# Optimization experiments

Hardware: AMD Instinct MI355X
Metric: run time of the kernel (lower is better)

## Reference

```python
import jax, jax.numpy as jnp
import numpy as np

N = 100000   # nodes
E = 1600000  # edges
D = 128      # input_dim
H = 128      # hidden_dim
G = 1000     # num graphs
C = 10       # output_dim
EPS = 1e-5   # BatchNorm eps


def setup_inputs() -> dict:
    key = jax.random.key(0)
    ks = jax.random.split(key, 16)
    inp = {
        "x": jax.random.normal(ks[0], (N, D), dtype=jnp.float32),
        "edge_index": jax.random.randint(ks[1], (2, E), 0, N, dtype=jnp.int64),
        "batch": jnp.sort(jax.random.randint(ks[2], (N,), 0, G, dtype=jnp.int64)),
    }
    s_in, s_h = 1.0 / np.sqrt(D), 1.0 / np.sqrt(H)
    inp["W1"] = jax.random.normal(ks[3], (D, H), jnp.float32) * s_in
    inp["b1"] = jnp.zeros((H,), jnp.float32)
    inp["W2"] = jax.random.normal(ks[4], (H, H), jnp.float32) * s_h
    inp["b2"] = jnp.zeros((H,), jnp.float32)
    inp["W3"] = jax.random.normal(ks[5], (H, H), jnp.float32) * s_h
    inp["b3"] = jnp.zeros((H,), jnp.float32)
    for i in range(1, 4):
        inp[f"g{i}"] = jnp.ones((H,), jnp.float32)
        inp[f"be{i}"] = jnp.zeros((H,), jnp.float32)
    inp["Wc1"] = jax.random.normal(ks[6], (H, H // 2), jnp.float32) * s_h
    inp["bc1"] = jnp.zeros((H // 2,), jnp.float32)
    inp["Wc2"] = jax.random.normal(ks[7], (H // 2, C), jnp.float32) * (1.0 / np.sqrt(H // 2))
    inp["bc2"] = jnp.zeros((C,), jnp.float32)
    return inp


def _edge_norm(edge_index, num_nodes):
    # PyG GCNConv default: add self-loops, symmetric D^-1/2 A D^-1/2 normalization
    loop = jnp.arange(num_nodes, dtype=edge_index.dtype)
    src = jnp.concatenate([edge_index[0], loop])
    dst = jnp.concatenate([edge_index[1], loop])
    deg = jax.ops.segment_sum(jnp.ones_like(dst, dtype=jnp.float32), dst,
                              num_segments=num_nodes)
    dinv = jnp.where(deg > 0, deg ** -0.5, 0.0)
    norm = dinv[src] * dinv[dst]  # [E + N]
    return src, dst, norm


def _gcn_conv(x, W, b, src, dst, norm, num_nodes):
    h = x @ W                              # [N, H]
    msg = h[src] * norm[:, None]           # gather over edges (incl. self-loops)
    out = jax.ops.segment_sum(msg, dst, num_segments=num_nodes)
    return out + b


def _bn_eval(x, gamma, beta):
    # eval-mode BatchNorm1d with running_mean=0, running_var=1 buffers
    return gamma * x * (1.0 / np.sqrt(1.0 + EPS)) + beta


def reference(x, edge_index, batch,
              W1, b1, W2, b2, W3, b3,
              g1, be1, g2, be2, g3, be3,
              Wc1, bc1, Wc2, bc2):
    num_nodes = x.shape[0]
    src, dst, norm = _edge_norm(edge_index, num_nodes)
    h = x
    for (W, b, g, be) in ((W1, b1, g1, be1), (W2, b2, g2, be2), (W3, b3, g3, be3)):
        h = _gcn_conv(h, W, b, src, dst, norm, num_nodes)
        h = jax.nn.relu(_bn_eval(h, g, be))  # dropout is identity in eval mode
    # global_mean_pool over graph ids
    sums = jax.ops.segment_sum(h, batch, num_segments=G)
    cnts = jax.ops.segment_sum(jnp.ones((num_nodes,), h.dtype), batch, num_segments=G)
    pooled = sums / jnp.maximum(cnts, 1.0)[:, None]
    # classifier MLP
    z = jax.nn.relu(pooled @ Wc1 + bc1)
    return z @ Wc2 + bc2
```

## Files before the change

### kernel.cpp

```cpp
#include <hip/hip_runtime.h>
#include <hip/hip_bf16.h>

#define INV1P 0.9999950000374997f
#define BCAP 16384
#define CSRCAP 20480

typedef __attribute__((ext_vector_type(8))) short bfrag;
typedef __attribute__((ext_vector_type(4))) float f32x4;

static __device__ __forceinline__ unsigned bf16rne(float f) {
    unsigned u = __float_as_uint(f);
    return (u + 0x7fffu + ((u >> 16) & 1u)) >> 16;
}
static __device__ __forceinline__ float bflo(unsigned u) { return __uint_as_float(u << 16); }
static __device__ __forceinline__ float bfhi(unsigned u) { return __uint_as_float(u & 0xffff0000u); }


__global__ __launch_bounds__(256) void k_binA(const int* __restrict__ src, const int* __restrict__ dst,
                                              int* __restrict__ gcursor, unsigned* __restrict__ binned, int e) {
    __shared__ unsigned pk[8192];
    __shared__ unsigned char bk[8192];
    __shared__ int hist[256];
    __shared__ int base[256];
    int tid = threadIdx.x;
    hist[tid] = 0;
    __syncthreads();
    int cbase = blockIdx.x * 8192;
    int cnt = min(8192, e - cbase);
    for (int j = tid; j < cnt; j += 256) {
        int s = src[cbase + j], d = dst[cbase + j];
        unsigned b = (unsigned)d >> 9;
        pk[j] = (unsigned)s | (((unsigned)d & 511u) << 17);
        bk[j] = (unsigned char)b;
        atomicAdd(&hist[b], 1);
    }
    __syncthreads();
    int h = hist[tid];
    base[tid] = (h > 0) ? atomicAdd(&gcursor[tid], h) : 0;
    hist[tid] = 0;
    __syncthreads();
    for (int j = tid; j < cnt; j += 256) {
        unsigned b = bk[j];
        int off = atomicAdd(&hist[b], 1);
        binned[base[b] + off] = pk[j];
    }
}

__global__ __launch_bounds__(256) void k_binB2(const unsigned* __restrict__ binned,
                                               const int* __restrict__ gcursor,
                                               int* __restrict__ rowptr, int* __restrict__ rowend,
                                               float* __restrict__ dinv,
                                               int* __restrict__ csr_src, int n, int dummy) {
    __shared__ int cur[512];
    __shared__ int lrp[512];
    __shared__ int ssum[256];
    int b = blockIdx.x, tid = threadIdx.x;
    int nstart = b << 9;
    int nn = min(512, n - nstart);
    int cntb = gcursor[b] - b * BCAP;
    int s0 = b * BCAP, s1 = s0 + cntb;
    int cb = b * CSRCAP;
    cur[tid] = 0; cur[tid + 256] = 0;
    __syncthreads();
    for (int j = s0 + tid; j < s1; j += 256)
        atomicAdd(&cur[(binned[j] >> 17) & 511], 1);
    __syncthreads();
    int c0 = cur[2 * tid], c1 = cur[2 * tid + 1];
    int p0 = (c0 + 7) & ~7, p1 = (c1 + 7) & ~7;
    int pair = p0 + p1;
    ssum[tid] = pair;
    __syncthreads();
    for (int off = 1; off < 256; off <<= 1) {
        int t2 = (tid >= off) ? ssum[tid - off] : 0;
        __syncthreads();
        ssum[tid] += t2;
        __syncthreads();
    }
    int e0 = ssum[tid] - pair;
    int e1 = e0 + p0;
    int st0 = cb + e0, st1 = cb + e1;
    lrp[2 * tid] = st0;
    lrp[2 * tid + 1] = st1;
    if (2 * tid < nn) {
        rowptr[nstart + 2 * tid] = st0;
        rowend[nstart + 2 * tid] = st0 + p0;
        dinv[nstart + 2 * tid] = rsqrtf((float)(c0 + 1));
    }
    if (2 * tid + 1 < nn) {
        rowptr[nstart + 2 * tid + 1] = st1;
        rowend[nstart + 2 * tid + 1] = st1 + p1;
        dinv[nstart + 2 * tid + 1] = rsqrtf((float)(c1 + 1));
    }
    for (int k = c0; k < p0; k++) csr_src[st0 + k] = dummy;
    for (int k = c1; k < p1; k++) csr_src[st1 + k] = dummy;
    cur[2 * tid] = 0; cur[2 * tid + 1] = 0;
    __syncthreads();
    for (int j = s0 + tid; j < s1; j += 256) {
        unsigned p = binned[j];
        int nl = (p >> 17) & 511;
        int idx = atomicAdd(&cur[nl], 1);
        csr_src[lrp[nl] + idx] = p & 0x1ffff;
    }
}


static __device__ __forceinline__ void prepw_body(const float* __restrict__ W, uint4* __restrict__ Bf, int blk) {
    int id = blk * 256 + threadIdx.x;
    int lane = id & 63;
    int e = id >> 6;
    int kk = e >> 3, c = e & 7;
    int kbase = kk * 32 + (lane >> 4) * 8;
    int col = c * 16 + (lane & 15);
    unsigned hi[8], lo[8];
    #pragma unroll
    for (int j = 0; j < 8; j++) {
        float w = W[(kbase + j) * 128 + col];
        unsigned h = bf16rne(w);
        float rh = __uint_as_float(h << 16);
        unsigned l = bf16rne(w - rh);
        hi[j] = h; lo[j] = l;
    }
    uint4 H = make_uint4(hi[0] | (hi[1] << 16), hi[2] | (hi[3] << 16),
                         hi[4] | (hi[5] << 16), hi[6] | (hi[7] << 16));
    uint4 L = make_uint4(lo[0] | (lo[1] << 16), lo[2] | (lo[3] << 16),
                         lo[4] | (lo[5] << 16), lo[6] | (lo[7] << 16));
    Bf[e * 64 + lane] = H;
    Bf[2048 + e * 64 + lane] = L;
}

__global__ __launch_bounds__(256) void k_prep(const float* __restrict__ W1, const float* __restrict__ W2,
                                              const float* __restrict__ W3,
                                              uint4* __restrict__ Bf1, uint4* __restrict__ Bf2,
                                              uint4* __restrict__ Bf3,
                                              int* __restrict__ gcursor,
                                              unsigned* __restrict__ bufA, unsigned* __restrict__ bufB, int n) {
    int b = blockIdx.x;
    if (b < 8)       prepw_body(W1, Bf1, b);
    else if (b < 16) prepw_body(W2, Bf2, b - 8);
    else if (b < 24) prepw_body(W3, Bf3, b - 16);
    else {
        int t = threadIdx.x;
        gcursor[t] = t * BCAP;
        if (t < 64)  bufA[(size_t)n * 64 + t] = 0;
        else if (t < 128) bufB[(size_t)n * 64 + (t - 64)] = 0;
    }
}

static __device__ __forceinline__ void gemm_body(unsigned* __restrict__ Y, const float* __restrict__ dinv,
                                                 int nrows, int rowbase, bfrag* a, uint4* bs) {
    int tid = threadIdx.x;
    int w = tid >> 6, lane = tid & 63;
    __syncthreads();
    f32x4 acc[8];
    #pragma unroll
    for (int c = 0; c < 8; c++) acc[c] = (f32x4){0.f, 0.f, 0.f, 0.f};
    #pragma unroll
    for (int kk = 0; kk < 4; kk++) {
        #pragma unroll
        for (int c = 0; c < 8; c++) {
            bfrag bh = *(const bfrag*)&bs[(kk * 8 + c) * 64 + lane];
            bfrag bl = *(const bfrag*)&bs[2048 + (kk * 8 + c) * 64 + lane];
            acc[c] = __builtin_amdgcn_mfma_f32_16x16x32_bf16(a[kk], bh, acc[c], 0, 0, 0);
            acc[c] = __builtin_amdgcn_mfma_f32_16x16x32_bf16(a[kk], bl, acc[c], 0, 0, 0);
        }
    }
    int rb = rowbase + w * 16 + (lane >> 4) * 4;
    float dv[4];
    #pragma unroll
    for (int r = 0; r < 4; r++) dv[r] = dinv[min(rb + r, nrows - 1)];
    __syncthreads();
    char* epib = (char*)bs;
    ushort* epi = (ushort*)(epib + w * 4352);
    #pragma unroll
    for (int c = 0; c < 8; c++) {
        #pragma unroll
        for (int r = 0; r < 4; r++) {
            int rr = (lane >> 4) * 4 + r;
            epi[rr * 136 + c * 16 + (lane & 15)] = (ushort)bf16rne(acc[c][r] * dv[r]);
        }
    }
    __syncthreads();
    #pragma unroll
    for (int i = 0; i < 4; i++) {
        int id = tid + i * 512;
        int rr = id >> 4, q = id & 15;
        int grow = rowbase + rr;
        if (grow < nrows) {
            uint4 v = *(const uint4*)(epib + (rr >> 4) * 4352 + (rr & 15) * 272 + q * 16);
            ((uint4*)Y)[(size_t)grow * 16 + q] = v;
        }
    }
}

__global__ __launch_bounds__(512) void k_gemm_mfma_f32(const float* __restrict__ X,
                                                       const uint4* __restrict__ Bfr,
                                                       unsigned* __restrict__ Y, const float* __restrict__ dinv,
                                                       int nrows) {
    __shared__ uint4 bs[4096];
    int tid = threadIdx.x;
    int w = tid >> 6, lane = tid & 63;
    int rowbase = blockIdx.x * 128;
    #pragma unroll
    for (int i = 0; i < 8; i++) bs[tid + i * 512] = Bfr[tid + i * 512];
    int row = rowbase + w * 16 + (lane & 15);
    int rowc = min(row, nrows - 1);
    const float4* X4 = (const float4*)X;
    bfrag a[4];
    #pragma unroll
    for (int kk = 0; kk < 4; kk++) {
        float4 f0 = X4[(size_t)rowc * 32 + kk * 8 + (lane >> 4) * 2];
        float4 f1 = X4[(size_t)rowc * 32 + kk * 8 + (lane >> 4) * 2 + 1];
        uint4 av = make_uint4(bf16rne(f0.x) | (bf16rne(f0.y) << 16),
                              bf16rne(f0.z) | (bf16rne(f0.w) << 16),
                              bf16rne(f1.x) | (bf16rne(f1.y) << 16),
                              bf16rne(f1.z) | (bf16rne(f1.w) << 16));
        a[kk] = *(const bfrag*)&av;
    }
    gemm_body(Y, dinv, nrows, rowbase, a, bs);
}

static __device__ __forceinline__ void agg_body(const uint4* __restrict__ H4, int nodec, int l,
                                                const int* __restrict__ rowptr, const int* __restrict__ rowend,
                                                const int* __restrict__ csr_src, float* acc) {
    {
        uint4 hv = H4[(size_t)nodec * 16 + l];
        acc[0] = bflo(hv.x); acc[1] = bfhi(hv.x);
        acc[2] = bflo(hv.y); acc[3] = bfhi(hv.y);
        acc[4] = bflo(hv.z); acc[5] = bfhi(hv.z);
        acc[6] = bflo(hv.w); acc[7] = bfhi(hv.w);
    }
    int s = rowptr[nodec], e = rowend[nodec];
    const int4* csr4 = (const int4*)csr_src;
    int4 ia, ib;
    if (s < e) {
        ia = csr4[(s >> 2)];
        ib = csr4[(s >> 2) + 1];
    }
    for (int j = s; j < e; j += 8) {
        uint4 vv[8];
        vv[0] = H4[(size_t)ia.x * 16 + l];
        vv[1] = H4[(size_t)ia.y * 16 + l];
        vv[2] = H4[(size_t)ia.z * 16 + l];
        vv[3] = H4[(size_t)ia.w * 16 + l];
        vv[4] = H4[(size_t)ib.x * 16 + l];
        vv[5] = H4[(size_t)ib.y * 16 + l];
        vv[6] = H4[(size_t)ib.z * 16 + l];
        vv[7] = H4[(size_t)ib.w * 16 + l];
        int jn = j + 8;
        if (jn < e) {
            ia = csr4[(jn >> 2)];
            ib = csr4[(jn >> 2) + 1];
        }
        #pragma unroll
        for (int q = 0; q < 8; q++) {
            acc[0] += bflo(vv[q].x); acc[1] += bfhi(vv[q].x);
            acc[2] += bflo(vv[q].y); acc[3] += bfhi(vv[q].y);
            acc[4] += bflo(vv[q].z); acc[5] += bfhi(vv[q].z);
            acc[6] += bflo(vv[q].w); acc[7] += bfhi(vv[q].w);
        }
    }
}

static __device__ __forceinline__ void bn_relu(const float* acc, float dn, int l,
                                               const float* __restrict__ bias, const float* __restrict__ gamma,
                                               const float* __restrict__ beta, float* r) {
    float4 bi0 = ((const float4*)bias)[l * 2],  bi1 = ((const float4*)bias)[l * 2 + 1];
    float4 ga0 = ((const float4*)gamma)[l * 2], ga1 = ((const float4*)gamma)[l * 2 + 1];
    float4 be0 = ((const float4*)beta)[l * 2],  be1 = ((const float4*)beta)[l * 2 + 1];
    float g[8] = {ga0.x, ga0.y, ga0.z, ga0.w, ga1.x, ga1.y, ga1.z, ga1.w};
    float bb[8] = {bi0.x, bi0.y, bi0.z, bi0.w, bi1.x, bi1.y, bi1.z, bi1.w};
    float bt[8] = {be0.x, be0.y, be0.z, be0.w, be1.x, be1.y, be1.z, be1.w};
    #pragma unroll
    for (int i = 0; i < 8; i++) {
        float t = g[i] * INV1P;
        r[i] = fmaxf(fmaf(t * dn, acc[i], fmaf(t, bb[i], bt[i])), 0.f);
    }
}

__global__ __launch_bounds__(256) void k_agg_gemm(const uint4* __restrict__ H4,
                                                  const int* __restrict__ rowptr, const int* __restrict__ rowend,
                                                  const int* __restrict__ csr_src,
                                                  const float* __restrict__ dinv,
                                                  const float* __restrict__ bias, const float* __restrict__ gamma,
                                                  const float* __restrict__ beta,
                                                  const uint4* __restrict__ Bfr,
                                                  unsigned* __restrict__ Yn, int nnodes) {
    __shared__ ushort hs[16 * 136];
    int tid = threadIdx.x;
    int nl = tid >> 4;
    int l = tid & 15;
    int base = blockIdx.x * 16;

    {
        int node = base + nl;
        int nodec = min(node, nnodes - 1);
        float acc[8], r[8];
        agg_body(H4, nodec, l, rowptr, rowend, csr_src, acc);
        bn_relu(acc, dinv[nodec], l, bias, gamma, beta, r);
        uint4 o;
        o.x = bf16rne(r[0]) | (bf16rne(r[1]) << 16);
        o.y = bf16rne(r[2]) | (bf16rne(r[3]) << 16);
        o.z = bf16rne(r[4]) | (bf16rne(r[5]) << 16);
        o.w = bf16rne(r[6]) | (bf16rne(r[7]) << 16);
        *(uint4*)&hs[nl * 136 + l * 8] = o;
    }
    __syncthreads();

    int w = tid >> 6, lane = tid & 63;
    int c0 = 2 * w, c1 = 2 * w + 1;
    bfrag a[4];
    #pragma unroll
    for (int kk = 0; kk < 4; kk++)
        a[kk] = *(const bfrag*)&hs[(lane & 15) * 136 + (lane >> 4) * 8 + kk * 32];
    f32x4 ac0 = (f32x4){0.f, 0.f, 0.f, 0.f};
    f32x4 ac1 = (f32x4){0.f, 0.f, 0.f, 0.f};
    #pragma unroll
    for (int kk = 0; kk < 4; kk++) {
        bfrag bh0 = *(const bfrag*)&Bfr[(kk * 8 + c0) * 64 + lane];
        bfrag bl0 = *(const bfrag*)&Bfr[2048 + (kk * 8 + c0) * 64 + lane];
        bfrag bh1 = *(const bfrag*)&Bfr[(kk * 8 + c1) * 64 + lane];
        bfrag bl1 = *(const bfrag*)&Bfr[2048 + (kk * 8 + c1) * 64 + lane];
        ac0 = __builtin_amdgcn_mfma_f32_16x16x32_bf16(a[kk], bh0, ac0, 0, 0, 0);
        ac0 = __builtin_amdgcn_mfma_f32_16x16x32_bf16(a[kk], bl0, ac0, 0, 0, 0);
        ac1 = __builtin_amdgcn_mfma_f32_16x16x32_bf16(a[kk], bh1, ac1, 0, 0, 0);
        ac1 = __builtin_amdgcn_mfma_f32_16x16x32_bf16(a[kk], bl1, ac1, 0, 0, 0);
    }
    __syncthreads();
    #pragma unroll
    for (int r = 0; r < 4; r++) {
        int rowt = (lane >> 4) * 4 + r;
        float dv = dinv[min(base + rowt, nnodes - 1)];
        hs[rowt * 136 + c0 * 16 + (lane & 15)] = (ushort)bf16rne(ac0[r] * dv);
        hs[rowt * 136 + c1 * 16 + (lane & 15)] = (ushort)bf16rne(ac1[r] * dv);
    }
    __syncthreads();
    {
        int row = tid >> 4, q = tid & 15;
        int grow = base + row;
        if (grow < nnodes)
            ((uint4*)Yn)[(size_t)grow * 16 + q] = *(const uint4*)&hs[row * 136 + q * 8];
    }
}

__global__ __launch_bounds__(256) void k_aggregate(const uint4* __restrict__ H4, const int* __restrict__ rowptr,
                                                   const int* __restrict__ rowend,
                                                   const int* __restrict__ csr_src,
                                                   const float* __restrict__ dinv,
                                                   const float* __restrict__ bias, const float* __restrict__ gamma,
                                                   const float* __restrict__ beta,
                                                   uint4* __restrict__ out4, int nnodes) {
    int tid = blockIdx.x * 256 + threadIdx.x;
    int node = tid >> 4;
    int l = tid & 15;
    if (node >= nnodes) return;
    float acc[8], r[8];
    agg_body(H4, node, l, rowptr, rowend, csr_src, acc);
    bn_relu(acc, dinv[node], l, bias, gamma, beta, r);
    uint4 o;
    o.x = bf16rne(r[0]) | (bf16rne(r[1]) << 16);
    o.y = bf16rne(r[2]) | (bf16rne(r[3]) << 16);
    o.z = bf16rne(r[4]) | (bf16rne(r[5]) << 16);
    o.w = bf16rne(r[6]) | (bf16rne(r[7]) << 16);
    out4[(size_t)node * 16 + l] = o;
}

__global__ __launch_bounds__(64) void k_pool(const unsigned* __restrict__ Hf, const int* __restrict__ batch,
                                             float* __restrict__ pooled, float* __restrict__ cnt, int nnodes) {
    int t = threadIdx.x;
    int base = blockIdx.x * 64;
    if (base >= nnodes) return;
    int end = min(base + 64, nnodes);
    float ax = 0.f, ay = 0.f; int run = 0;
    int cur = batch[base];
    for (int i = base; i < end; i++) {
        int bg = batch[i];
        if (bg != cur) {
            atomicAdd(&pooled[(size_t)cur * 128 + 2 * t], ax);
            atomicAdd(&pooled[(size_t)cur * 128 + 2 * t + 1], ay);
            if (t == 0) atomicAdd(&cnt[cur], (float)run);
            ax = 0.f; ay = 0.f; run = 0; cur = bg;
        }
        unsigned u = Hf[(size_t)i * 64 + t];
        ax += bflo(u);
        ay += bfhi(u);
        run++;
    }
    atomicAdd(&pooled[(size_t)cur * 128 + 2 * t], ax);
    atomicAdd(&pooled[(size_t)cur * 128 + 2 * t + 1], ay);
    if (t == 0) atomicAdd(&cnt[cur], (float)run);
}

__global__ __launch_bounds__(64) void k_classifier(const float* __restrict__ pooled, const float* __restrict__ cnt,
                                                   const float* __restrict__ Wc1, const float* __restrict__ bc1,
                                                   const float* __restrict__ Wc2, const float* __restrict__ bc2,
                                                   float* __restrict__ outp, int ngraphs) {
    __shared__ float p[128];
    __shared__ float z[64];
    int g = blockIdx.x;
    int tid = threadIdx.x;
    float inv = 1.0f / fmaxf(cnt[g], 1.0f);
    p[tid]      = pooled[(size_t)g * 128 + tid] * inv;
    p[tid + 64] = pooled[(size_t)g * 128 + 64 + tid] * inv;
    __syncthreads();
    float a = bc1[tid];
    #pragma unroll 8
    for (int k = 0; k < 128; k++) a += p[k] * Wc1[k * 64 + tid];
    z[tid] = fmaxf(a, 0.f);
    __syncthreads();
    if (tid < 10) {
        float o = bc2[tid];
        #pragma unroll 8
        for (int j = 0; j < 64; j++) o += z[j] * Wc2[j * 10 + tid];
        outp[(size_t)g * 10 + tid] = o;
    }
}


static inline size_t align16(size_t v) { return (v + 15) & ~(size_t)15; }

extern "C" void kernel_launch(void* const* d_in, const int* in_sizes, int n_in,
                              void* d_out, int out_size, void* d_ws, size_t ws_size,
                              hipStream_t stream) {
    const float* x      = (const float*)d_in[0];
    const int*   ei     = (const int*)d_in[1];
    const int*   batch  = (const int*)d_in[2];
    const float* W1 = (const float*)d_in[3];  const float* b1 = (const float*)d_in[4];
    const float* W2 = (const float*)d_in[5];  const float* b2 = (const float*)d_in[6];
    const float* W3 = (const float*)d_in[7];  const float* b3 = (const float*)d_in[8];
    const float* g1 = (const float*)d_in[9];  const float* be1 = (const float*)d_in[10];
    const float* g2 = (const float*)d_in[11]; const float* be2 = (const float*)d_in[12];
    const float* g3 = (const float*)d_in[13]; const float* be3 = (const float*)d_in[14];
    const float* Wc1 = (const float*)d_in[15]; const float* bc1 = (const float*)d_in[16];
    const float* Wc2 = (const float*)d_in[17]; const float* bc2 = (const float*)d_in[18];

    const int N = in_sizes[0] / 128;
    const int E = in_sizes[1] / 2;
    const int G = out_size / 10;
    const int* srcp = ei;
    const int* dstp = ei + E;
    const int NB = (N + 511) >> 9;

    char* ws = (char*)d_ws;
    size_t off = 0;
    unsigned* bufA = (unsigned*)(ws + off); off = align16(off + (size_t)(N + 1) * 64 * 4);
    unsigned* bufB = (unsigned*)(ws + off); off = align16(off + (size_t)(N + 1) * 64 * 4);
    uint4* Bfr1 = (uint4*)(ws + off); off = align16(off + 4096 * 16);
    uint4* Bfr2 = (uint4*)(ws + off); off = align16(off + 4096 * 16);
    uint4* Bfr3 = (uint4*)(ws + off); off = align16(off + 4096 * 16);
    int*   csr_src = (int*)(ws + off);  off = align16(off + (size_t)NB * CSRCAP * 4);
    unsigned* binned = (unsigned*)(ws + off); off = align16(off + (size_t)NB * BCAP * 4);
    float* dinv   = (float*)(ws + off); off = align16(off + (size_t)N * 4);
    int*   rowptr = (int*)(ws + off);   off = align16(off + (size_t)N * 4);
    int*   rowend = (int*)(ws + off);   off = align16(off + (size_t)N * 4);
    int*   gcursor = (int*)(ws + off);  off = align16(off + 256 * 4);
    float* pooled = (float*)(ws + off); off = align16(off + (size_t)G * 128 * 4);
    float* cnt    = (float*)(ws + off); off = align16(off + (size_t)G * 4);
    (void)ws_size;

    int gE8 = (E + 8191) / 8192;

    k_prep<<<25, 256, 0, stream>>>(W1, W2, W3, Bfr1, Bfr2, Bfr3, gcursor, bufA, bufB, N);

    k_binA<<<gE8, 256, 0, stream>>>(srcp, dstp, gcursor, binned, E);
    k_binB2<<<NB, 256, 0, stream>>>(binned, gcursor, rowptr, rowend, dinv, csr_src, N, N);

    int gGemm = (N + 127) / 128;
    int gFuse = (N + 15) / 16;
    int gAgg  = (N * 16 + 255) / 256;

    k_gemm_mfma_f32<<<gGemm, 512, 0, stream>>>(x, Bfr1, bufA, dinv, N);
    k_agg_gemm<<<gFuse, 256, 0, stream>>>((const uint4*)bufA, rowptr, rowend, csr_src, dinv,
                                          b1, g1, be1, Bfr2, bufB, N);
    k_agg_gemm<<<gFuse, 256, 0, stream>>>((const uint4*)bufB, rowptr, rowend, csr_src, dinv,
                                          b2, g2, be2, Bfr3, bufA, N);
    k_aggregate<<<gAgg, 256, 0, stream>>>((const uint4*)bufA, rowptr, rowend, csr_src, dinv,
                                          b3, g3, be3, (uint4*)bufB, N);

    hipMemsetAsync(pooled, 0, ((size_t)G * 128 + G) * 4, stream);
    int gPool = (N + 63) / 64;
    k_pool<<<gPool, 64, 0, stream>>>(bufB, batch, pooled, cnt, N);

    k_classifier<<<G, 64, 0, stream>>>(pooled, cnt, Wc1, bc1, Wc2, bc2, (float*)d_out, G);
}
```

Measured before the change: 286.8 us.

## Fuse final aggregation with mean pooling and widen agg-gemm blocks to 32 nodes

The last aggregation kernel now pools its outputs directly: each 16-node block stages fp32 results in shared memory and issues one atomicAdd per graph segment. This removes the bf16 write and re-read of the final hidden layer and one kernel launch. Separately, the fused aggregate+GEMM kernel now handles 32 nodes per 512-thread block, so each wave reuses its B fragments across two 16-row tiles. The cost is more pooled atomics, since segments are split every 16 nodes instead of every 64, plus higher LDS and register use per block.

```diff
diff --git a/kernel.cpp b/kernel.cpp
--- a/kernel.cpp
+++ b/kernel.cpp
@@ -277,7 +277,7 @@
     }
 }
 
-__global__ __launch_bounds__(256) void k_agg_gemm(const uint4* __restrict__ H4,
+__global__ __launch_bounds__(512) void k_agg_gemm(const uint4* __restrict__ H4,
                                                   const int* __restrict__ rowptr, const int* __restrict__ rowend,
                                                   const int* __restrict__ csr_src,
                                                   const float* __restrict__ dinv,
@@ -285,11 +285,11 @@
                                                   const float* __restrict__ beta,
                                                   const uint4* __restrict__ Bfr,
                                                   unsigned* __restrict__ Yn, int nnodes) {
-    __shared__ ushort hs[16 * 136];
+    __shared__ ushort hs[32 * 136];
     int tid = threadIdx.x;
     int nl = tid >> 4;
     int l = tid & 15;
-    int base = blockIdx.x * 16;
+    int base = blockIdx.x * 32;
 
     {
         int node = base + nl;
@@ -307,31 +307,31 @@
     __syncthreads();
 
     int w = tid >> 6, lane = tid & 63;
-    int c0 = 2 * w, c1 = 2 * w + 1;
-    bfrag a[4];
-    #pragma unroll
-    for (int kk = 0; kk < 4; kk++)
-        a[kk] = *(const bfrag*)&hs[(lane & 15) * 136 + (lane >> 4) * 8 + kk * 32];
+    bfrag a0[4], a1[4];
+    #pragma unroll
+    for (int kk = 0; kk < 4; kk++) {
+        a0[kk] = *(const bfrag*)&hs[(lane & 15) * 136 + (lane >> 4) * 8 + kk * 32];
+        a1[kk] = *(const bfrag*)&hs[(16 + (lane & 15)) * 136 + (lane >> 4) * 8 + kk * 32];
+    }
     f32x4 ac0 = (f32x4){0.f, 0.f, 0.f, 0.f};
     f32x4 ac1 = (f32x4){0.f, 0.f, 0.f, 0.f};
     #pragma unroll
     for (int kk = 0; kk < 4; kk++) {
-        bfrag bh0 = *(const bfrag*)&Bfr[(kk * 8 + c0) * 64 + lane];
-        bfrag bl0 = *(const bfrag*)&Bfr[2048 + (kk * 8 + c0) * 64 + lane];
-        bfrag bh1 = *(const bfrag*)&Bfr[(kk * 8 + c1) * 64 + lane];
-        bfrag bl1 = *(const bfrag*)&Bfr[2048 + (kk * 8 + c1) * 64 + lane];
-        ac0 = __builtin_amdgcn_mfma_f32_16x16x32_bf16(a[kk], bh0, ac0, 0, 0, 0);
-        ac0 = __builtin_amdgcn_mfma_f32_16x16x32_bf16(a[kk], bl0, ac0, 0, 0, 0);
-        ac1 = __builtin_amdgcn_mfma_f32_16x16x32_bf16(a[kk], bh1, ac1, 0, 0, 0);
-        ac1 = __builtin_amdgcn_mfma_f32_16x16x32_bf16(a[kk], bl1, ac1, 0, 0, 0);
+        bfrag bh = *(const bfrag*)&Bfr[(kk * 8 + w) * 64 + lane];
+        bfrag bl = *(const bfrag*)&Bfr[2048 + (kk * 8 + w) * 64 + lane];
+        ac0 = __builtin_amdgcn_mfma_f32_16x16x32_bf16(a0[kk], bh, ac0, 0, 0, 0);
+        ac0 = __builtin_amdgcn_mfma_f32_16x16x32_bf16(a0[kk], bl, ac0, 0, 0, 0);
+        ac1 = __builtin_amdgcn_mfma_f32_16x16x32_bf16(a1[kk], bh, ac1, 0, 0, 0);
+        ac1 = __builtin_amdgcn_mfma_f32_16x16x32_bf16(a1[kk], bl, ac1, 0, 0, 0);
     }
     __syncthreads();
     #pragma unroll
     for (int r = 0; r < 4; r++) {
         int rowt = (lane >> 4) * 4 + r;
-        float dv = dinv[min(base + rowt, nnodes - 1)];
-        hs[rowt * 136 + c0 * 16 + (lane & 15)] = (ushort)bf16rne(ac0[r] * dv);
-        hs[rowt * 136 + c1 * 16 + (lane & 15)] = (ushort)bf16rne(ac1[r] * dv);
+        float dv0 = dinv[min(base + rowt, nnodes - 1)];
+        float dv1 = dinv[min(base + 16 + rowt, nnodes - 1)];
+        hs[rowt * 136 + w * 16 + (lane & 15)] = (ushort)bf16rne(ac0[r] * dv0);
+        hs[(16 + rowt) * 136 + w * 16 + (lane & 15)] = (ushort)bf16rne(ac1[r] * dv1);
     }
     __syncthreads();
     {
@@ -342,52 +342,61 @@
     }
 }
 
-__global__ __launch_bounds__(256) void k_aggregate(const uint4* __restrict__ H4, const int* __restrict__ rowptr,
-                                                   const int* __restrict__ rowend,
-                                                   const int* __restrict__ csr_src,
-                                                   const float* __restrict__ dinv,
-                                                   const float* __restrict__ bias, const float* __restrict__ gamma,
-                                                   const float* __restrict__ beta,
-                                                   uint4* __restrict__ out4, int nnodes) {
-    int tid = blockIdx.x * 256 + threadIdx.x;
-    int node = tid >> 4;
+__global__ __launch_bounds__(256) void k_agg_pool(const uint4* __restrict__ H4, const int* __restrict__ rowptr,
+                                                  const int* __restrict__ rowend,
+                                                  const int* __restrict__ csr_src,
+                                                  const float* __restrict__ dinv,
+                                                  const float* __restrict__ bias, const float* __restrict__ gamma,
+                                                  const float* __restrict__ beta,
+                                                  const int* __restrict__ batch,
+                                                  float* __restrict__ pooled, float* __restrict__ cnt,
+                                                  int nnodes) {
+    __shared__ float hsf[16 * 132];
+    __shared__ int bg[16];
+    int tid = threadIdx.x;
+    int nl = tid >> 4;
     int l = tid & 15;
-    if (node >= nnodes) return;
-    float acc[8], r[8];
-    agg_body(H4, node, l, rowptr, rowend, csr_src, acc);
-    bn_relu(acc, dinv[node], l, bias, gamma, beta, r);
-    uint4 o;
-    o.x = bf16rne(r[0]) | (bf16rne(r[1]) << 16);
-    o.y = bf16rne(r[2]) | (bf16rne(r[3]) << 16);
-    o.z = bf16rne(r[4]) | (bf16rne(r[5]) << 16);
-    o.w = bf16rne(r[6]) | (bf16rne(r[7]) << 16);
-    out4[(size_t)node * 16 + l] = o;
-}
-
-__global__ __launch_bounds__(64) void k_pool(const unsigned* __restrict__ Hf, const int* __restrict__ batch,
-                                             float* __restrict__ pooled, float* __restrict__ cnt, int nnodes) {
-    int t = threadIdx.x;
-    int base = blockIdx.x * 64;
-    if (base >= nnodes) return;
-    int end = min(base + 64, nnodes);
-    float ax = 0.f, ay = 0.f; int run = 0;
-    int cur = batch[base];
-    for (int i = base; i < end; i++) {
-        int bg = batch[i];
-        if (bg != cur) {
-            atomicAdd(&pooled[(size_t)cur * 128 + 2 * t], ax);
-            atomicAdd(&pooled[(size_t)cur * 128 + 2 * t + 1], ay);
-            if (t == 0) atomicAdd(&cnt[cur], (float)run);
-            ax = 0.f; ay = 0.f; run = 0; cur = bg;
-        }
-        unsigned u = Hf[(size_t)i * 64 + t];
-        ax += bflo(u);
-        ay += bfhi(u);
-        run++;
-    }
-    atomicAdd(&pooled[(size_t)cur * 128 + 2 * t], ax);
-    atomicAdd(&pooled[(size_t)cur * 128 + 2 * t + 1], ay);
-    if (t == 0) atomicAdd(&cnt[cur], (float)run);
+    int base = blockIdx.x * 16;
+    int nn = min(16, nnodes - base);
+
+    if (tid < 16) bg[tid] = batch[min(base + tid, nnodes - 1)];
+
+    {
+        int node = base + nl;
+        int nodec = min(node, nnodes - 1);
+        float acc[8], r[8];
+        agg_body(H4, nodec, l, rowptr, rowend, csr_src, acc);
+        bn_relu(acc, dinv[nodec], l, bias, gamma, beta, r);
+        #pragma unroll
+        for (int i = 0; i < 8; i++) hsf[nl * 132 + l * 8 + i] = r[i];
+    }
+    __syncthreads();
+
+    if (tid < 128) {
+        float ax = 0.f;
+        int curg = bg[0];
+        for (int i = 0; i < nn; i++) {
+            int g = bg[i];
+            if (g != curg) {
+                atomicAdd(&pooled[(size_t)curg * 128 + tid], ax);
+                ax = 0.f; curg = g;
+            }
+            ax += hsf[i * 132 + tid];
+        }
+        if (nn > 0) atomicAdd(&pooled[(size_t)curg * 128 + tid], ax);
+    } else if (tid == 128) {
+        float run = 0.f;
+        int curg = bg[0];
+        for (int i = 0; i < nn; i++) {
+            int g = bg[i];
+            if (g != curg) {
+                atomicAdd(&cnt[curg], run);
+                run = 0.f; curg = g;
+            }
+            run += 1.f;
+        }
+        if (nn > 0) atomicAdd(&cnt[curg], run);
+    }
 }
 
 __global__ __launch_bounds__(64) void k_classifier(const float* __restrict__ pooled, const float* __restrict__ cnt,
@@ -459,26 +468,23 @@
 
     int gE8 = (E + 8191) / 8192;
 
+    hipMemsetAsync(pooled, 0, ((size_t)G * 128 + G) * 4, stream);
     k_prep<<<25, 256, 0, stream>>>(W1, W2, W3, Bfr1, Bfr2, Bfr3, gcursor, bufA, bufB, N);
 
     k_binA<<<gE8, 256, 0, stream>>>(srcp, dstp, gcursor, binned, E);
     k_binB2<<<NB, 256, 0, stream>>>(binned, gcursor, rowptr, rowend, dinv, csr_src, N, N);
 
     int gGemm = (N + 127) / 128;
-    int gFuse = (N + 15) / 16;
-    int gAgg  = (N * 16 + 255) / 256;
+    int gFuse = (N + 31) / 32;
+    int gFin  = (N + 15) / 16;
 
     k_gemm_mfma_f32<<<gGemm, 512, 0, stream>>>(x, Bfr1, bufA, dinv, N);
-    k_agg_gemm<<<gFuse, 256, 0, stream>>>((const uint4*)bufA, rowptr, rowend, csr_src, dinv,
+    k_agg_gemm<<<gFuse, 512, 0, stream>>>((const uint4*)bufA, rowptr, rowend, csr_src, dinv,
                                           b1, g1, be1, Bfr2, bufB, N);
-    k_agg_gemm<<<gFuse, 256, 0, stream>>>((const uint4*)bufB, rowptr, rowend, csr_src, dinv,
+    k_agg_gemm<<<gFuse, 512, 0, stream>>>((const uint4*)bufB, rowptr, rowend, csr_src, dinv,
                                           b2, g2, be2, Bfr3, bufA, N);
-    k_aggregate<<<gAgg, 256, 0, stream>>>((const uint4*)bufA, rowptr, rowend, csr_src, dinv,
-                                          b3, g3, be3, (uint4*)bufB, N);
-
-    hipMemsetAsync(pooled, 0, ((size_t)G * 128 + G) * 4, stream);
-    int gPool = (N + 63) / 64;
-    k_pool<<<gPool, 64, 0, stream>>>(bufB, batch, pooled, cnt, N);
+    k_agg_pool<<<gFin, 256, 0, stream>>>((const uint4*)bufA, rowptr, rowend, csr_src, dinv,
+                                         b3, g3, be3, batch, pooled, cnt, N);
 
     k_classifier<<<G, 64, 0, stream>>>(pooled, cnt, Wc1, bc1, Wc2, bc2, (float*)d_out, G);
 }
```

New measurement: 266.2 us. -7.2%, faster.
